# Performance work log

Measured on AMD Instinct MI355X. Metric: run time of the kernel, lower is better.

## Reference

```python
import jax, jax.numpy as jnp
import numpy as np

EPS = 1e-5

def _ternary_ste(w):
    # STEQuantize: round(w/scale) clamped to [-1,1]; straight-through gradient.
    scale = jnp.maximum(jnp.mean(jnp.abs(w)), EPS)
    q = jnp.clip(jnp.round(w / scale), -1.0, 1.0)
    return w + jax.lax.stop_gradient(q - w)

def _bitlinear(x, w):
    # BitLinear: y = x @ (ternary(w) * scale)^T, scale = mean|w| (differentiable).
    scale = jnp.maximum(jnp.mean(jnp.abs(w)), EPS)
    return x @ (_ternary_ste(w) * scale).T

def _op_library(x, indices, weights, ops):
    # ops: (n_ops, D, D). Per-op ternary quantize + scale, then one batched einsum
    # instead of the python loop of small matmuls.
    n_ops = ops.shape[0]
    scales = jnp.maximum(jnp.mean(jnp.abs(ops), axis=(1, 2)), EPS)  # (n_ops,)
    q = jnp.clip(jnp.round(ops / scales[:, None, None]), -1.0, 1.0)
    w_eff = (ops + jax.lax.stop_gradient(q - ops)) * scales[:, None, None]  # (n,o,d)
    # transformed[n] = x @ w_eff[n]^T  ->  (B, S, n_ops, D)
    T = jnp.einsum('bsd,nod->bsno', x, w_eff)
    out = (1e-5 / n_ops) * jnp.sum(T, axis=2)
    gathered = jnp.take_along_axis(T, indices[:, :, :, None], axis=2)  # (B,S,K,D)
    out = out + jnp.sum(weights[..., None] * gathered, axis=2)
    return out

def _mem_read(x, slots, W_read):
    d = slots.shape[1]
    key = x @ W_read.T
    attn = jax.nn.softmax(key @ slots.T / jnp.sqrt(jnp.float32(d)), axis=-1)
    return attn @ slots

def _layernorm(x, gamma, beta):
    mu = jnp.mean(x, axis=-1, keepdims=True)
    var = jnp.var(x, axis=-1, keepdims=True)
    return (x - mu) * jax.lax.rsqrt(var + EPS) * gamma + beta

def _single_pass(reason, ops, W_router, slots, W_read, W_mix, ln_gamma, ln_beta, top_k):
    logits = _bitlinear(reason, W_router)              # (B,S,n_ops)
    vals, indices = jax.lax.top_k(logits, top_k)       # (B,S,K)
    weights = jax.nn.softmax(vals, axis=-1)
    op_out = _op_library(reason, indices, weights, ops)
    mem_out = _mem_read(reason, slots, W_read)
    mixed = jnp.concatenate([op_out, mem_out], axis=-1) @ W_mix.T
    return _layernorm(reason + mixed, ln_gamma, ln_beta)

def _write_signal(q, slots, W_wk, W_wg, W_wv):
    d = slots.shape[1]
    wk = q @ W_wk.T
    wg = jax.nn.sigmoid(q @ W_wg.T)                    # (B,S,1)
    wv = q @ W_wv.T
    addr = jax.nn.softmax(wk @ slots.T / jnp.sqrt(jnp.float32(d)), axis=-1)
    return wg * wv + 0.1 * (addr @ slots)

def setup_inputs() -> dict:
    key = jax.random.key(0)
    ks = jax.random.split(key, 12)
    B, S, d_model, d_reason = 8, 2048, 1024, 128
    n_ops, n_slots = 32, 16
    return {
        'hidden': jax.random.normal(ks[0], (B, S, d_model), jnp.float32),
        'force_depth': 2,
        'W_down': jax.random.normal(ks[1], (d_reason, d_model), jnp.float32) * 0.02,
        'W_up': jax.random.normal(ks[2], (d_model, d_reason), jnp.float32) * 0.02,
        'ops': jax.random.normal(ks[3], (n_ops, d_reason, d_reason), jnp.float32) * 0.02,
        'W_router': jax.random.normal(ks[4], (n_ops, d_reason), jnp.float32) * 0.02,
        'slots': jax.random.normal(ks[5], (n_slots, d_reason), jnp.float32) * 0.01,
        'W_read': jax.random.normal(ks[6], (d_reason, d_reason), jnp.float32) * 0.02,
        'W_wk': jax.random.normal(ks[7], (d_reason, d_reason), jnp.float32) * 0.02,
        'W_wg': jax.random.normal(ks[8], (1, d_reason), jnp.float32) * 0.02,
        'W_wv': jax.random.normal(ks[9], (d_reason, d_reason), jnp.float32) * 0.02,
        'W_mix': jax.random.normal(ks[10], (d_reason, 2 * d_reason), jnp.float32) * 0.02,
        'ln_gamma': jnp.ones((d_reason,), jnp.float32),
        'ln_beta': jnp.zeros((d_reason,), jnp.float32),
        'write_scale': jnp.float32(0.01),
    }

def reference(hidden, force_depth, W_down, W_up, ops, W_router, slots, W_read,
              W_wk, W_wg, W_wv, W_mix, ln_gamma, ln_beta, write_scale):
    top_k = 2
    reason = _bitlinear(hidden, W_down)
    for _ in range(int(force_depth)):
        reason = _single_pass(reason, ops, W_router, slots, W_read, W_mix,
                              ln_gamma, ln_beta, top_k)
    reason = reason + write_scale * _write_signal(reason, slots, W_wk, W_wg, W_wv)
    out = _bitlinear(reason, W_up)
    return hidden + out
```

## Files before the change

kernel.cpp:

```cpp
#include <hip/hip_runtime.h>


#define DR   128
#define DM   1024
#define NTOK 16384
#define NOPS 32
#define COEF (1e-5f / 32.f)

typedef __attribute__((ext_vector_type(8))) short bfrag;
typedef __attribute__((ext_vector_type(4))) float f32x4;

__device__ __forceinline__ ushort f2b_bits(float f) {
  union { float f; uint i; } c; c.f = f;
  uint x = c.i;
  return (ushort)((x + 0x7fffu + ((x >> 16) & 1u)) >> 16);
}
__device__ __forceinline__ float qeff(float w, float s) {
  float q = rintf(w / s);
  q = fminf(1.f, fmaxf(-1.f, q));
  return q * s;
}
__device__ __forceinline__ float waveRed(float v) {
#pragma unroll
  for (int m = 32; m > 0; m >>= 1) v += __shfl_xor(v, m, 64);
  return v;
}

#define OFF_SUMS    0
#define OFF_OPSSC   256
#define OFF_WDE     512
#define OFF_WUE     (OFF_WDE + 262144)
#define OFF_WRT     (OFF_WUE + 262144)
#define OFF_OPSB    (OFF_WRT + 16384)
#define OFF_WMIXA   (OFF_OPSB + 1048576)
#define OFF_WWVB    (OFF_WMIXA + 32768)
#define OFF_MRS     (OFF_WWVB + 32768)
#define OFF_MWS     (OFF_MRS + 8192)
#define OFF_SB      (OFF_MWS + 8192)
#define OFF_SLOTS   (OFF_SB + 8192)
#define OFF_WWG     (OFF_SLOTS + 8192)
#define OFF_GAMMA   (OFF_WWG + 512)
#define OFF_BETA    (OFF_GAMMA + 512)
#define OFF_WSC     (OFF_BETA + 512)
#define OFF_RF      (OFF_WSC + 256)
#define WS_TOTAL    (OFF_RF + 4194304)

__global__ __launch_bounds__(1024) void k_absum_all(
    const float* __restrict__ W_down, const float* __restrict__ W_router,
    const float* __restrict__ W_up, const float* __restrict__ ops,
    float* __restrict__ sums) {
  __shared__ float ws16[16];
  const int y = blockIdx.x;
  const int tid = threadIdx.x;
  const float* src; int n;
  if (y == 0)      { src = W_down;   n = 131072; }
  else if (y == 1) { src = W_router; n = 4096;   }
  else if (y == 2) { src = W_up;     n = 131072; }
  else             { src = ops + (size_t)(y - 3) * 16384; n = 16384; }
  float s = 0.f;
  for (int i = tid * 4; i < n; i += 4096) {
    float4 v = *(const float4*)(src + i);
    s += fabsf(v.x) + fabsf(v.y) + fabsf(v.z) + fabsf(v.w);
  }
  s = waveRed(s);
  const int lane = tid & 63, wv = tid >> 6;
  if (lane == 0) ws16[wv] = s;
  __syncthreads();
  if (tid == 0) {
    float t = 0.f;
#pragma unroll
    for (int i = 0; i < 16; ++i) t += ws16[i];
    sums[y] = t;
  }
}

__global__ __launch_bounds__(256) void k_build(
    const float* __restrict__ W_down, const float* __restrict__ W_up,
    const float* __restrict__ W_router, const float* __restrict__ ops,
    const float* __restrict__ W_read, const float* __restrict__ W_wk,
    const float* __restrict__ W_wg, const float* __restrict__ W_wv,
    const float* __restrict__ W_mix, const float* __restrict__ slots,
    const float* __restrict__ gamma, const float* __restrict__ beta,
    const float* __restrict__ wscale, int has_wsc, const float* __restrict__ sums,
    ushort* __restrict__ WdE, ushort* __restrict__ WuE, float* __restrict__ WrT,
    ushort* __restrict__ opsB, float* __restrict__ opsScale,
    ushort* __restrict__ WmixA, ushort* __restrict__ WwvB,
    float* __restrict__ Mrs, float* __restrict__ Mws, float* __restrict__ SBw,
    float* __restrict__ slotsF, float* __restrict__ WwgF,
    float* __restrict__ gammaF, float* __restrict__ betaF, float* __restrict__ wscF) {
  int id = blockIdx.x * 256 + threadIdx.x;
  const float s_wd = fmaxf(sums[0] * (1.f / 131072.f), 1e-5f);
  const float s_wr = fmaxf(sums[1] * (1.f / 4096.f), 1e-5f);
  const float s_wu = fmaxf(sums[2] * (1.f / 131072.f), 1e-5f);

  if (id < 131072) { WdE[id] = f2b_bits(qeff(W_down[id], s_wd)); return; }
  id -= 131072;
  if (id < 131072) { WuE[id] = f2b_bits(qeff(W_up[id], s_wu)); return; }
  id -= 131072;
  if (id < 4096) {
    int d = id >> 5, n = id & 31;
    WrT[id] = qeff(W_router[n * DR + d], s_wr);
    return;
  }
  id -= 4096;
  if (id < 524288) {
    int n = id >> 14;
    float s = fmaxf(sums[3 + n] * (1.f / 16384.f), 1e-5f);
    float q = rintf(ops[id] / s);
    q = fminf(1.f, fmaxf(-1.f, q));
    opsB[id] = f2b_bits(q);
    return;
  }
  id -= 524288;
  if (id < 32) { opsScale[id] = fmaxf(sums[3 + id] * (1.f / 16384.f), 1e-5f); return; }
  id -= 32;
  if (id < 16384) {
    int r = id >> 7, o = id & 127;
    WmixA[id] = f2b_bits(W_mix[r * 256 + o]);
    return;
  }
  id -= 16384;
  if (id < 16384) { WwvB[id] = f2b_bits(W_wv[id]); return; }
  id -= 16384;
  if (id < 2048) {
    int d = id >> 4, j = id & 15;
    float a = 0.f;
#pragma unroll 8
    for (int o = 0; o < DR; ++o) a += W_read[o * DR + d] * slots[j * DR + o];
    Mrs[id] = a;
    return;
  }
  id -= 2048;
  if (id < 2048) {
    int d = id >> 4, j = id & 15;
    float a = 0.f;
#pragma unroll 8
    for (int o = 0; o < DR; ++o) a += W_wk[o * DR + d] * slots[j * DR + o];
    Mws[id] = a;
    return;
  }
  id -= 2048;
  if (id < 2048) {
    int j = id >> 7, r = id & 127;
    float a = 0.f;
#pragma unroll 8
    for (int o = 0; o < DR; ++o) a += slots[j * DR + o] * W_mix[r * 256 + 128 + o];
    SBw[id] = a;
    return;
  }
  id -= 2048;
  if (id < 2048) { slotsF[id] = slots[id]; return; }
  id -= 2048;
  if (id < 128) { WwgF[id] = W_wg[id]; return; }
  id -= 128;
  if (id < 128) { gammaF[id] = gamma[id]; return; }
  id -= 128;
  if (id < 128) { betaF[id] = beta[id]; return; }
  id -= 128;
  if (id == 0) { wscF[0] = has_wsc ? wscale[0] : 0.01f; }
}

__global__ __launch_bounds__(256) void k_down(const float* __restrict__ hidden,
                                              const ushort* __restrict__ WdE,
                                              float* __restrict__ X) {
  const int w = threadIdx.x >> 6, lane = threadIdx.x & 63;
  const int quad = lane >> 4, mrow = lane & 15;
  const int m0 = blockIdx.x * 16;
  const int c0 = w * 32;

  f32x4 acc[2];
  acc[0] = (f32x4){0.f, 0.f, 0.f, 0.f};
  acc[1] = (f32x4){0.f, 0.f, 0.f, 0.f};

  const float* Ap = hidden + (size_t)(m0 + mrow) * DM + quad * 8;
#pragma unroll 2
  for (int kt = 0; kt < 32; ++kt) {
    float4 a0 = *(const float4*)(Ap + kt * 32);
    float4 a1 = *(const float4*)(Ap + kt * 32 + 4);
    bfrag a;
    a[0] = (short)f2b_bits(a0.x); a[1] = (short)f2b_bits(a0.y);
    a[2] = (short)f2b_bits(a0.z); a[3] = (short)f2b_bits(a0.w);
    a[4] = (short)f2b_bits(a1.x); a[5] = (short)f2b_bits(a1.y);
    a[6] = (short)f2b_bits(a1.z); a[7] = (short)f2b_bits(a1.w);
#pragma unroll
    for (int nt = 0; nt < 2; ++nt) {
      bfrag b = *(const bfrag*)(WdE + (size_t)(c0 + nt * 16 + mrow) * DM + kt * 32 + quad * 8);
      acc[nt] = __builtin_amdgcn_mfma_f32_16x16x32_bf16(a, b, acc[nt], 0, 0, 0);
    }
  }
#pragma unroll
  for (int nt = 0; nt < 2; ++nt)
#pragma unroll
    for (int r = 0; r < 4; ++r)
      X[(size_t)(m0 + quad * 4 + r) * DR + c0 + nt * 16 + mrow] = acc[nt][r];
}

__global__ __launch_bounds__(512) void k_pass2(
    float* __restrict__ X, ushort* __restrict__ RF, int emit,
    const float* __restrict__ WrT, const ushort* __restrict__ opsB,
    const float* __restrict__ opsScale, const ushort* __restrict__ WmixA,
    const float* __restrict__ Mrs, const float* __restrict__ SBw,
    const float* __restrict__ gammaF, const float* __restrict__ betaF,
    const ushort* __restrict__ WwvB, const float* __restrict__ Mws,
    const float* __restrict__ slotsF, const float* __restrict__ WwgF,
    const float* __restrict__ wscF) {
  __shared__ float  xsf[64][132];
  __shared__ ushort xsb[64][136];
  __shared__ float  lg[64][33];
  __shared__ float  coefT[32][64];
  __shared__ float  attn[64][17];
  __shared__ float  at2[64][17];
  __shared__ float  WrTs[4096];
  __shared__ float  Mrss[2048];
  __shared__ float  Mwss[2048];
  __shared__ float  SBws[2048];
  __shared__ float  slotss[2048];
  __shared__ int    seli[64][2];
  __shared__ float  selw[64][2];
  __shared__ float  gp[64];
  __shared__ float  partS[8][4][4];
  __shared__ float  partQ[8][4][4];

  const int tid = threadIdx.x;
  const int w = tid >> 6, lane = tid & 63;
  const int quad = lane >> 4, mrow = lane & 15;
  const int t0 = blockIdx.x * 64;

  {
    float4* d;
    const float4* s;
    d = (float4*)WrTs; s = (const float4*)WrT;
    for (int i = tid; i < 1024; i += 512) d[i] = s[i];
    ((float4*)Mrss)[tid]   = ((const float4*)Mrs)[tid];
    ((float4*)Mwss)[tid]   = ((const float4*)Mws)[tid];
    ((float4*)SBws)[tid]   = ((const float4*)SBw)[tid];
    ((float4*)slotss)[tid] = ((const float4*)slotsF)[tid];
  }
  for (int i = tid; i < 2048; i += 512) {
    float4 v = *(const float4*)(X + (size_t)t0 * DR + i * 4);
    int t = i >> 5, c = (i & 31) * 4;
    xsf[t][c] = v.x; xsf[t][c + 1] = v.y; xsf[t][c + 2] = v.z; xsf[t][c + 3] = v.w;
    xsb[t][c] = f2b_bits(v.x); xsb[t][c + 1] = f2b_bits(v.y);
    xsb[t][c + 2] = f2b_bits(v.z); xsb[t][c + 3] = f2b_bits(v.w);
  }
  __syncthreads();

  for (int p = tid; p < 2048; p += 512) {
    int t = p >> 5, n = p & 31;
    const float4* xr = (const float4*)&xsf[t][0];
    float a = 0.f;
#pragma unroll 8
    for (int d4 = 0; d4 < 32; ++d4) {
      float4 x = xr[d4];
      a += x.x * WrTs[(d4 * 4 + 0) * 32 + n];
      a += x.y * WrTs[(d4 * 4 + 1) * 32 + n];
      a += x.z * WrTs[(d4 * 4 + 2) * 32 + n];
      a += x.w * WrTs[(d4 * 4 + 3) * 32 + n];
    }
    lg[t][n] = a;
  }
  for (int p = tid; p < 1024; p += 512) {
    int t = p >> 4, j = p & 15;
    const float4* xr = (const float4*)&xsf[t][0];
    float a = 0.f;
#pragma unroll 8
    for (int d4 = 0; d4 < 32; ++d4) {
      float4 x = xr[d4];
      a += x.x * Mrss[(d4 * 4 + 0) * 16 + j];
      a += x.y * Mrss[(d4 * 4 + 1) * 16 + j];
      a += x.z * Mrss[(d4 * 4 + 2) * 16 + j];
      a += x.w * Mrss[(d4 * 4 + 3) * 16 + j];
    }
    attn[t][j] = a * 0.088388347648318447f;
  }
  __syncthreads();

  if (tid < 64) {
    float v0 = -1e30f; int i0 = 0;
#pragma unroll
    for (int n = 0; n < 32; ++n) { float v = lg[tid][n]; if (v > v0) { v0 = v; i0 = n; } }
    float v1 = -1e30f; int i1 = 0;
#pragma unroll
    for (int n = 0; n < 32; ++n)
      if (n != i0) { float v = lg[tid][n]; if (v > v1) { v1 = v; i1 = n; } }
    float e = expf(v1 - v0);
    float w0 = 1.f / (1.f + e);
    seli[tid][0] = i0; seli[tid][1] = i1;
    selw[tid][0] = w0; selw[tid][1] = e * w0;
  } else if (tid < 128) {
    const int t = tid - 64;
    float m = -1e30f;
#pragma unroll
    for (int j = 0; j < 16; ++j) m = fmaxf(m, attn[t][j]);
    float s = 0.f;
#pragma unroll
    for (int j = 0; j < 16; ++j) { float ee = expf(attn[t][j] - m); attn[t][j] = ee; s += ee; }
    float inv = 1.f / s;
#pragma unroll
    for (int j = 0; j < 16; ++j) attn[t][j] *= inv;
  }
  __syncthreads();

  for (int p = tid; p < 2048; p += 512) {
    int n = p >> 6, t = p & 63;
    float cf = COEF;
    if (n == seli[t][0]) cf += selw[t][0];
    if (n == seli[t][1]) cf += selw[t][1];
    coefT[n][t] = cf * opsScale[n];
  }
  __syncthreads();

  bfrag a[4][4];
#pragma unroll
  for (int m = 0; m < 4; ++m)
#pragma unroll
    for (int kt = 0; kt < 4; ++kt)
      a[m][kt] = *(const bfrag*)&xsb[m * 16 + mrow][kt * 32 + quad * 8];

  const ushort* Bp = opsB + (size_t)(w * 16 + mrow) * DR + quad * 8;
  bfrag bc[4], bn[4];
#pragma unroll
  for (int kt = 0; kt < 4; ++kt) bc[kt] = *(const bfrag*)(Bp + kt * 32);

  f32x4 out[4];
#pragma unroll
  for (int m = 0; m < 4; ++m) out[m] = (f32x4){0.f, 0.f, 0.f, 0.f};

  for (int n = 0; n < NOPS; ++n) {
    if (n + 1 < NOPS) {
      const ushort* Bn = Bp + (size_t)(n + 1) * (DR * DR);
#pragma unroll
      for (int kt = 0; kt < 4; ++kt) bn[kt] = *(const bfrag*)(Bn + kt * 32);
    }
    f32x4 tmp[4];
#pragma unroll
    for (int m = 0; m < 4; ++m) tmp[m] = (f32x4){0.f, 0.f, 0.f, 0.f};
#pragma unroll
    for (int kt = 0; kt < 4; ++kt)
#pragma unroll
      for (int m = 0; m < 4; ++m)
        tmp[m] = __builtin_amdgcn_mfma_f32_16x16x32_bf16(a[m][kt], bc[kt], tmp[m], 0, 0, 0);
#pragma unroll
    for (int m = 0; m < 4; ++m) {
      f32x4 cf = *(const f32x4*)&coefT[n][m * 16 + quad * 4];
      out[m] += cf * tmp[m];
    }
    if (n + 1 < NOPS) {
#pragma unroll
      for (int kt = 0; kt < 4; ++kt) bc[kt] = bn[kt];
    }
  }
  __syncthreads();

#pragma unroll
  for (int m = 0; m < 4; ++m)
#pragma unroll
    for (int r = 0; r < 4; ++r)
      xsb[m * 16 + quad * 4 + r][w * 16 + mrow] = f2b_bits(out[m][r]);
  __syncthreads();

  const int mtile = w & 3;
  const int ch = (w >> 2) * 64;
  {
    bfrag a2[4];
#pragma unroll
    for (int kt = 0; kt < 4; ++kt)
      a2[kt] = *(const bfrag*)&xsb[mtile * 16 + mrow][kt * 32 + quad * 8];

    f32x4 acc[4];
#pragma unroll
    for (int i = 0; i < 4; ++i) acc[i] = (f32x4){0.f, 0.f, 0.f, 0.f};
#pragma unroll
    for (int kt = 0; kt < 4; ++kt)
#pragma unroll
      for (int nt = 0; nt < 4; ++nt) {
        bfrag b = *(const bfrag*)(WmixA + (size_t)(ch + nt * 16 + mrow) * DR + kt * 32 + quad * 8);
        acc[nt] = __builtin_amdgcn_mfma_f32_16x16x32_bf16(a2[kt], b, acc[nt], 0, 0, 0);
      }

    float v[4][4];
#pragma unroll
    for (int nt = 0; nt < 4; ++nt) {
      const int col = ch + nt * 16 + mrow;
#pragma unroll
      for (int r = 0; r < 4; ++r) {
        const int t = mtile * 16 + quad * 4 + r;
        float y0 = 0.f;
#pragma unroll
        for (int j = 0; j < 16; ++j) y0 += attn[t][j] * SBws[j * 128 + col];
        v[nt][r] = acc[nt][r] + xsf[t][col] + y0;
      }
    }
    float s[4], q[4];
#pragma unroll
    for (int r = 0; r < 4; ++r) {
      float ps = 0.f, pq = 0.f;
#pragma unroll
      for (int nt = 0; nt < 4; ++nt) { ps += v[nt][r]; pq += v[nt][r] * v[nt][r]; }
      s[r] = ps; q[r] = pq;
    }
#pragma unroll
    for (int m = 1; m < 16; m <<= 1)
#pragma unroll
      for (int r = 0; r < 4; ++r) {
        s[r] += __shfl_xor(s[r], m, 64);
        q[r] += __shfl_xor(q[r], m, 64);
      }
    if (mrow == 0)
#pragma unroll
      for (int r = 0; r < 4; ++r) { partS[w][quad][r] = s[r]; partQ[w][quad][r] = q[r]; }
    __syncthreads();

    float mu[4], rsd[4];
#pragma unroll
    for (int r = 0; r < 4; ++r) {
      float ts = s[r] + partS[w ^ 4][quad][r];
      float tq = q[r] + partQ[w ^ 4][quad][r];
      mu[r] = ts * (1.f / DR);
      float var = tq * (1.f / DR) - mu[r] * mu[r];
      rsd[r] = rsqrtf(var + 1e-5f);
    }
    if (!emit) {
#pragma unroll
      for (int nt = 0; nt < 4; ++nt) {
        const int col = ch + nt * 16 + mrow;
        const float g = gammaF[col], bb = betaF[col];
#pragma unroll
        for (int r = 0; r < 4; ++r) {
          const int t = mtile * 16 + quad * 4 + r;
          X[(size_t)(t0 + t) * DR + col] = (v[nt][r] - mu[r]) * rsd[r] * g + bb;
        }
      }
      return;
    }
#pragma unroll
    for (int nt = 0; nt < 4; ++nt) {
      const int col = ch + nt * 16 + mrow;
      const float g = gammaF[col], bb = betaF[col];
#pragma unroll
      for (int r = 0; r < 4; ++r) {
        const int t = mtile * 16 + quad * 4 + r;
        float val = (v[nt][r] - mu[r]) * rsd[r] * g + bb;
        xsf[t][col] = val;
        xsb[t][col] = f2b_bits(val);
      }
    }
  }
  __syncthreads();

  for (int p = tid; p < 1024; p += 512) {
    int t = p >> 4, j = p & 15;
    const float4* xr = (const float4*)&xsf[t][0];
    float a2 = 0.f;
#pragma unroll 8
    for (int d4 = 0; d4 < 32; ++d4) {
      float4 x = xr[d4];
      a2 += x.x * Mwss[(d4 * 4 + 0) * 16 + j];
      a2 += x.y * Mwss[(d4 * 4 + 1) * 16 + j];
      a2 += x.z * Mwss[(d4 * 4 + 2) * 16 + j];
      a2 += x.w * Mwss[(d4 * 4 + 3) * 16 + j];
    }
    at2[t][j] = a2 * 0.088388347648318447f;
  }
  __syncthreads();

  if (tid < 64) {
    const float4* xr = (const float4*)&xsf[tid][0];
    float z = 0.f;
#pragma unroll 8
    for (int d4 = 0; d4 < 32; ++d4) {
      float4 x = xr[d4];
      z += x.x * WwgF[d4 * 4 + 0] + x.y * WwgF[d4 * 4 + 1]
         + x.z * WwgF[d4 * 4 + 2] + x.w * WwgF[d4 * 4 + 3];
    }
    gp[tid] = wscF[0] / (1.f + expf(-z));
  } else if (tid < 128) {
    const int t = tid - 64;
    float m = -1e30f;
#pragma unroll
    for (int j = 0; j < 16; ++j) m = fmaxf(m, at2[t][j]);
    float s = 0.f;
#pragma unroll
    for (int j = 0; j < 16; ++j) { float e = expf(at2[t][j] - m); at2[t][j] = e; s += e; }
    float inv = 1.f / s;
#pragma unroll
    for (int j = 0; j < 16; ++j) at2[t][j] *= inv;
  }
  __syncthreads();

  {
    bfrag a2[4];
#pragma unroll
    for (int kt = 0; kt < 4; ++kt)
      a2[kt] = *(const bfrag*)&xsb[mtile * 16 + mrow][kt * 32 + quad * 8];

    f32x4 acc[4];
#pragma unroll
    for (int i = 0; i < 4; ++i) acc[i] = (f32x4){0.f, 0.f, 0.f, 0.f};
#pragma unroll
    for (int kt = 0; kt < 4; ++kt)
#pragma unroll
      for (int nt = 0; nt < 4; ++nt) {
        bfrag b = *(const bfrag*)(WwvB + (size_t)(ch + nt * 16 + mrow) * DR + kt * 32 + quad * 8);
        acc[nt] = __builtin_amdgcn_mfma_f32_16x16x32_bf16(a2[kt], b, acc[nt], 0, 0, 0);
      }

    const float c01 = wscF[0] * 0.1f;
#pragma unroll
    for (int nt = 0; nt < 4; ++nt) {
      const int col = ch + nt * 16 + mrow;
#pragma unroll
      for (int r = 0; r < 4; ++r) {
        const int t = mtile * 16 + quad * 4 + r;
        float mo = 0.f;
#pragma unroll
        for (int j = 0; j < 16; ++j) mo += at2[t][j] * slotss[j * DR + col];
        float val = xsf[t][col] + gp[t] * acc[nt][r] + c01 * mo;
        RF[(size_t)(t0 + t) * DR + col] = f2b_bits(val);
      }
    }
  }
}

__global__ __launch_bounds__(256) void k_up(const ushort* __restrict__ Rf,
                                            const ushort* __restrict__ WuE,
                                            const float* __restrict__ hidden,
                                            float* __restrict__ out) {
  __shared__ float cs[64][132];

  const int wave = threadIdx.x >> 6, lane = threadIdx.x & 63;
  const int quad = lane >> 4, mrow = lane & 15;
  const int mt = blockIdx.x >> 3, ngrp = blockIdx.x & 7;
  const int m0b = mt * 64;
  const int m0 = m0b + wave * 16;
  const int c0 = ngrp * 128;

  f32x4 acc[8];
#pragma unroll
  for (int i = 0; i < 8; ++i) acc[i] = (f32x4){0.f, 0.f, 0.f, 0.f};

  const ushort* Ap = Rf + (size_t)(m0 + mrow) * DR + quad * 8;
#pragma unroll
  for (int kt = 0; kt < 4; ++kt) {
    bfrag a = *(const bfrag*)(Ap + kt * 32);
#pragma unroll
    for (int nt = 0; nt < 8; ++nt) {
      const ushort* Bp = WuE + (size_t)(c0 + nt * 16 + mrow) * DR + kt * 32 + quad * 8;
      bfrag b = *(const bfrag*)Bp;
      acc[nt] = __builtin_amdgcn_mfma_f32_16x16x32_bf16(a, b, acc[nt], 0, 0, 0);
    }
  }
#pragma unroll
  for (int nt = 0; nt < 8; ++nt)
#pragma unroll
    for (int r = 0; r < 4; ++r)
      cs[wave * 16 + quad * 4 + r][nt * 16 + mrow] = acc[nt][r];
  __syncthreads();

#pragma unroll
  for (int k = 0; k < 8; ++k) {
    const int i = threadIdx.x + k * 256;
    const int t = i >> 5, c4 = (i & 31) * 4;
    const size_t idx = (size_t)(m0b + t) * DM + c0 + c4;
    float4 h = *(const float4*)(hidden + idx);
    float4 v;
    v.x = h.x + cs[t][c4];
    v.y = h.y + cs[t][c4 + 1];
    v.z = h.z + cs[t][c4 + 2];
    v.w = h.w + cs[t][c4 + 3];
    *(float4*)(out + idx) = v;
  }
}

extern "C" void kernel_launch(void* const* d_in, const int* in_sizes, int n_in,
                              void* d_out, int out_size, void* d_ws, size_t ws_size,
                              hipStream_t stream) {
  int ns[20]; int nn = 0; int lastsc = -1;
  for (int i = 0; i < n_in; ++i) {
    if (in_sizes[i] == 1) lastsc = i;
    else if (nn < 20) ns[nn++] = i;
  }
  int iH = 0, iWd = 2, iWu = 3, iOps = 4, iWr = 5, iSl = 6, iRe = 7,
      iWk = 8, iWg = 9, iWv = 10, iMx = 11, iG = 12, iB = 13;
  if (nn >= 13) {
    iH  = ns[0];  iWd = ns[1];  iWu = ns[2];  iOps = ns[3]; iWr = ns[4];
    iSl = ns[5];  iRe = ns[6];  iWk = ns[7];  iWg = ns[8];  iWv = ns[9];
    iMx = ns[10]; iG  = ns[11]; iB  = ns[12];
  }
  const float* hidden   = (const float*)d_in[iH];
  const float* W_down   = (const float*)d_in[iWd];
  const float* W_up     = (const float*)d_in[iWu];
  const float* opsw     = (const float*)d_in[iOps];
  const float* W_router = (const float*)d_in[iWr];
  const float* slots    = (const float*)d_in[iSl];
  const float* W_read   = (const float*)d_in[iRe];
  const float* W_wk     = (const float*)d_in[iWk];
  const float* W_wg     = (const float*)d_in[iWg];
  const float* W_wv     = (const float*)d_in[iWv];
  const float* W_mix    = (const float*)d_in[iMx];
  const float* lng      = (const float*)d_in[iG];
  const float* lnb      = (const float*)d_in[iB];
  const float* wscale   = (lastsc >= 0) ? (const float*)d_in[lastsc] : (const float*)d_in[iG];
  const int has_wsc     = (lastsc >= 0) ? 1 : 0;

  char* ws = (char*)d_ws;
  float*  sums   = (float*)(ws + OFF_SUMS);
  float*  opsSc  = (float*)(ws + OFF_OPSSC);
  ushort* WdE    = (ushort*)(ws + OFF_WDE);
  ushort* WuE    = (ushort*)(ws + OFF_WUE);
  float*  WrT    = (float*)(ws + OFF_WRT);
  ushort* opsB   = (ushort*)(ws + OFF_OPSB);
  ushort* WmixA  = (ushort*)(ws + OFF_WMIXA);
  ushort* WwvB   = (ushort*)(ws + OFF_WWVB);
  float*  Mrs    = (float*)(ws + OFF_MRS);
  float*  Mws    = (float*)(ws + OFF_MWS);
  float*  SBw    = (float*)(ws + OFF_SB);
  float*  slotsF = (float*)(ws + OFF_SLOTS);
  float*  WwgF   = (float*)(ws + OFF_WWG);
  float*  gammaF = (float*)(ws + OFF_GAMMA);
  float*  betaF  = (float*)(ws + OFF_BETA);
  float*  wscF   = (float*)(ws + OFF_WSC);
  ushort* RF     = (ushort*)(ws + OFF_RF);

  float* X = (float*)d_out;

  k_absum_all<<<35, 1024, 0, stream>>>(W_down, W_router, W_up, opsw, sums);
  k_build<<<3250, 256, 0, stream>>>(W_down, W_up, W_router, opsw, W_read, W_wk, W_wg,
                                    W_wv, W_mix, slots, lng, lnb, wscale, has_wsc,
                                    sums, WdE, WuE, WrT, opsB, opsSc, WmixA, WwvB,
                                    Mrs, Mws, SBw, slotsF, WwgF, gammaF, betaF, wscF);
  k_down<<<1024, 256, 0, stream>>>(hidden, WdE, X);
  k_pass2<<<256, 512, 0, stream>>>(X, RF, 0, WrT, opsB, opsSc, WmixA, Mrs, SBw,
                                   gammaF, betaF, WwvB, Mws, slotsF, WwgF, wscF);
  k_pass2<<<256, 512, 0, stream>>>(X, RF, 1, WrT, opsB, opsSc, WmixA, Mrs, SBw,
                                   gammaF, betaF, WwvB, Mws, slotsF, WwgF, wscF);
  k_up<<<2048, 256, 0, stream>>>(RF, WuE, hidden, X);
}
```

Baseline: 365.2 us.

## Retile down-projection GEMM with LDS-staged bf16 activation tiles

```diff
diff --git a/kernel.cpp b/kernel.cpp
--- a/kernel.cpp
+++ b/kernel.cpp
@@ -160,39 +160,44 @@
   if (id == 0) { wscF[0] = has_wsc ? wscale[0] : 0.01f; }
 }
 
-__global__ __launch_bounds__(256) void k_down(const float* __restrict__ hidden,
+__global__ __launch_bounds__(512) void k_down(const float* __restrict__ hidden,
                                               const ushort* __restrict__ WdE,
                                               float* __restrict__ X) {
-  const int w = threadIdx.x >> 6, lane = threadIdx.x & 63;
+  __shared__ ushort stg[64][136];
+
+  const int tid = threadIdx.x;
+  const int w = tid >> 6, lane = tid & 63;
   const int quad = lane >> 4, mrow = lane & 15;
-  const int m0 = blockIdx.x * 16;
-  const int c0 = w * 32;
-
-  f32x4 acc[2];
-  acc[0] = (f32x4){0.f, 0.f, 0.f, 0.f};
-  acc[1] = (f32x4){0.f, 0.f, 0.f, 0.f};
-
-  const float* Ap = hidden + (size_t)(m0 + mrow) * DM + quad * 8;
-#pragma unroll 2
-  for (int kt = 0; kt < 32; ++kt) {
-    float4 a0 = *(const float4*)(Ap + kt * 32);
-    float4 a1 = *(const float4*)(Ap + kt * 32 + 4);
-    bfrag a;
-    a[0] = (short)f2b_bits(a0.x); a[1] = (short)f2b_bits(a0.y);
-    a[2] = (short)f2b_bits(a0.z); a[3] = (short)f2b_bits(a0.w);
-    a[4] = (short)f2b_bits(a1.x); a[5] = (short)f2b_bits(a1.y);
-    a[6] = (short)f2b_bits(a1.z); a[7] = (short)f2b_bits(a1.w);
-#pragma unroll
-    for (int nt = 0; nt < 2; ++nt) {
-      bfrag b = *(const bfrag*)(WdE + (size_t)(c0 + nt * 16 + mrow) * DM + kt * 32 + quad * 8);
-      acc[nt] = __builtin_amdgcn_mfma_f32_16x16x32_bf16(a, b, acc[nt], 0, 0, 0);
-    }
-  }
-#pragma unroll
-  for (int nt = 0; nt < 2; ++nt)
+  const int t0 = blockIdx.x * 64;
+
+  f32x4 dacc[4];
+#pragma unroll
+  for (int m = 0; m < 4; ++m) dacc[m] = (f32x4){0.f, 0.f, 0.f, 0.f};
+
+  for (int kc = 0; kc < 8; ++kc) {
+    for (int i = tid; i < 2048; i += 512) {
+      int t = i >> 5, c = (i & 31) * 4;
+      float4 v = *(const float4*)(hidden + (size_t)(t0 + t) * DM + kc * 128 + c);
+      stg[t][c] = f2b_bits(v.x); stg[t][c + 1] = f2b_bits(v.y);
+      stg[t][c + 2] = f2b_bits(v.z); stg[t][c + 3] = f2b_bits(v.w);
+    }
+    __syncthreads();
+#pragma unroll
+    for (int kt = 0; kt < 4; ++kt) {
+      bfrag b = *(const bfrag*)(WdE + (size_t)(w * 16 + mrow) * DM + kc * 128 + kt * 32 + quad * 8);
+#pragma unroll
+      for (int m = 0; m < 4; ++m) {
+        bfrag a = *(const bfrag*)&stg[m * 16 + mrow][kt * 32 + quad * 8];
+        dacc[m] = __builtin_amdgcn_mfma_f32_16x16x32_bf16(a, b, dacc[m], 0, 0, 0);
+      }
+    }
+    __syncthreads();
+  }
+#pragma unroll
+  for (int m = 0; m < 4; ++m)
 #pragma unroll
     for (int r = 0; r < 4; ++r)
-      X[(size_t)(m0 + quad * 4 + r) * DR + c0 + nt * 16 + mrow] = acc[nt][r];
+      X[(size_t)(t0 + m * 16 + quad * 4 + r) * DR + w * 16 + mrow] = dacc[m][r];
 }
 
 __global__ __launch_bounds__(512) void k_pass2(
@@ -629,7 +634,7 @@
                                     W_wv, W_mix, slots, lng, lnb, wscale, has_wsc,
                                     sums, WdE, WuE, WrT, opsB, opsSc, WmixA, WwvB,
                                     Mrs, Mws, SBw, slotsF, WwgF, gammaF, betaF, wscF);
-  k_down<<<1024, 256, 0, stream>>>(hidden, WdE, X);
+  k_down<<<256, 512, 0, stream>>>(hidden, WdE, X);
   k_pass2<<<256, 512, 0, stream>>>(X, RF, 0, WrT, opsB, opsSc, WmixA, Mrs, SBw,
                                    gammaF, betaF, WwvB, Mws, slotsF, WwgF, wscF);
   k_pass2<<<256, 512, 0, stream>>>(X, RF, 1, WrT, opsB, opsSc, WmixA, Mrs, SBw,
```

Result: faster. 344.0 us (-5.8%).
